# Kernel optimization log

Hardware: AMD Instinct MI355X
Metric: run time of the kernel (lower is better)

Reference implementation:

```python
import jax, jax.numpy as jnp
import numpy as np

NUM_HEADS = 16
HIDDEN = 1024
HEAD = HIDDEN // NUM_HEADS

def setup_inputs() -> dict:
    key = jax.random.key(0)
    k1, k2 = jax.random.split(key)
    embeddings = jax.random.normal(k1, (4, 2048, HIDDEN), dtype=jnp.float32)
    w_qkv = jax.random.normal(k2, (HIDDEN, 3 * HIDDEN), dtype=jnp.float32) * (1.0 / np.sqrt(HIDDEN))
    return {"embeddings": embeddings, "w_qkv": w_qkv}

def reference(embeddings, w_qkv):
    b, s, h = embeddings.shape
    # qkv projection (no bias): [b, s, 3*h]
    result = embeddings @ w_qkv
    # split '(qkv nah hdsz)': qkv outermost, then heads, then head dim
    result = result.reshape(b, s, 3, NUM_HEADS, HEAD)
    q = jnp.transpose(result[:, :, 0], (0, 2, 1, 3))  # [b, nah, s, hd]
    k = jnp.transpose(result[:, :, 1], (0, 2, 1, 3))
    v = jnp.transpose(result[:, :, 2], (0, 2, 1, 3))
    # NOTE: original scales by 1/sqrt(hidden_size), not 1/sqrt(head_size)
    scores = jnp.einsum('bnqd,bnkd->bnqk', q, k) / jnp.sqrt(jnp.float32(h))
    probs = jax.nn.softmax(scores, axis=-1)
    ctx = jnp.einsum('bnqk,bnkd->bnqd', probs, v)  # [b, nah, s, hd]
    out = jnp.transpose(ctx, (0, 2, 1, 3)).reshape(b, s, h)
    return out
```

## Files before the change

### kernel.cpp

```cpp
#include <hip/hip_runtime.h>
#include <hip/hip_bf16.h>


typedef __attribute__((ext_vector_type(8))) __bf16 bf16x8;
typedef __attribute__((ext_vector_type(8))) unsigned short u16x8;
typedef __attribute__((ext_vector_type(4))) unsigned short u16x4;
typedef __attribute__((ext_vector_type(4))) float f32x4;

#define B_  4
#define S_  2048
#define H_  1024
#define NH_ 16
#define HD_ 64
#define N3_ 3072
#define M_  (B_*S_)

static __device__ __forceinline__ unsigned short f2bf(float f) {
  __bf16 h = (__bf16)f;
  return __builtin_bit_cast(unsigned short, h);
}

__global__ __launch_bounds__(256) void cvt_emb_kernel(
    const float* __restrict__ in, unsigned short* __restrict__ out, int n4) {
  int i = blockIdx.x * blockDim.x + threadIdx.x;
  int stride = gridDim.x * blockDim.x;
  const float4* in4 = (const float4*)in;
  for (; i < n4; i += stride) {
    float4 v = in4[i];
    ushort4 o;
    o.x = f2bf(v.x); o.y = f2bf(v.y); o.z = f2bf(v.z); o.w = f2bf(v.w);
    ((ushort4*)out)[i] = o;
  }
}

__global__ __launch_bounds__(256) void cvt_w_kernel(
    const float* __restrict__ in, unsigned short* __restrict__ out) {
  __shared__ __align__(16) unsigned short tile[64 * 64];
  const int t = threadIdx.x;
  const int n0 = blockIdx.x * 64;
  const int k0 = blockIdx.y * 64;
#pragma unroll
  for (int it = 0; it < 4; ++it) {
    int c = it * 256 + t;
    int row = c >> 4;
    int a = c & 15;
    float4 v = *(const float4*)(in + (size_t)(k0 + row) * N3_ + n0 + a * 4);
    u16x4 o;
    o[0] = f2bf(v.x); o[1] = f2bf(v.y); o[2] = f2bf(v.z); o[3] = f2bf(v.w);
    int swz = (((row & 7) ^ ((row >> 3) & 7)) << 4);
    *(u16x4*)((char*)tile + row * 128 + ((a * 8) ^ swz)) = o;
  }
  __syncthreads();
#pragma unroll
  for (int it = 0; it < 2; ++it) {
    int c = it * 256 + t;
    int n = c >> 3;
    int a = c & 7;
    u16x8 o;
#pragma unroll
    for (int j = 0; j < 8; ++j) {
      int k = a * 8 + j;
      int swz = (((k & 7) ^ ((k >> 3) & 7)) << 4);
      o[j] = *(const unsigned short*)((char*)tile + k * 128 + ((2 * n) ^ swz));
    }
    *(u16x8*)(out + (size_t)(n0 + n) * H_ + k0 + a * 8) = o;
  }
}

__global__ __launch_bounds__(256) void qkv_gemm_kernel(
    const unsigned short* __restrict__ A,
    const unsigned short* __restrict__ BT,
    unsigned short* __restrict__ C) {
  __shared__ __align__(16) unsigned short a_lds[128 * 64];
  __shared__ __align__(16) unsigned short b_lds[128 * 64];
  const int t = threadIdx.x;
  const int lane = t & 63;
  const int w = t >> 6;
  const int wm = w >> 1, wn = w & 1;
  const int m0 = blockIdx.y * 128;
  const int n0 = blockIdx.x * 128;
  const int lr = lane & 15;
  const int lh = lane >> 4;

  f32x4 acc[4][4];
  for (int i = 0; i < 4; i++)
    for (int j = 0; j < 4; j++)
      for (int r = 0; r < 4; r++) acc[i][j][r] = 0.f;

  for (int kt = 0; kt < 16; ++kt) {
    __syncthreads();
#pragma unroll
    for (int r = 0; r < 4; ++r) {
      int idx = r * 256 + t;
      int row = idx >> 3, ch = idx & 7;
      int sw = (ch * 16) ^ ((row & 7) << 4);
      u16x8 av = *(const u16x8*)(A + (size_t)(m0 + row) * H_ + kt * 64 + ch * 8);
      *(u16x8*)((char*)a_lds + row * 128 + sw) = av;
      u16x8 bv = *(const u16x8*)(BT + (size_t)(n0 + row) * H_ + kt * 64 + ch * 8);
      *(u16x8*)((char*)b_lds + row * 128 + sw) = bv;
    }
    __syncthreads();
#pragma unroll
    for (int kb = 0; kb < 2; ++kb) {
      bf16x8 af[4], bfr[4];
#pragma unroll
      for (int mi = 0; mi < 4; mi++) {
        int row = wm * 64 + mi * 16 + lr;
        int off = (kb * 64 + lh * 16) ^ ((row & 7) << 4);
        af[mi] = *(const bf16x8*)((char*)a_lds + row * 128 + off);
      }
#pragma unroll
      for (int ni = 0; ni < 4; ni++) {
        int row = wn * 64 + ni * 16 + lr;
        int off = (kb * 64 + lh * 16) ^ ((row & 7) << 4);
        bfr[ni] = *(const bf16x8*)((char*)b_lds + row * 128 + off);
      }
#pragma unroll
      for (int mi = 0; mi < 4; mi++)
#pragma unroll
        for (int ni = 0; ni < 4; ni++)
          acc[mi][ni] = __builtin_amdgcn_mfma_f32_16x16x32_bf16(
              af[mi], bfr[ni], acc[mi][ni], 0, 0, 0);
    }
  }
#pragma unroll
  for (int mi = 0; mi < 4; mi++)
#pragma unroll
    for (int ni = 0; ni < 4; ni++)
#pragma unroll
      for (int rg = 0; rg < 4; rg++) {
        int row = m0 + wm * 64 + mi * 16 + lh * 4 + rg;
        int col = n0 + wn * 64 + ni * 16 + lr;
        C[(size_t)row * N3_ + col] = f2bf(acc[mi][ni][rg]);
      }
}

__global__ __launch_bounds__(256) void vtrans_kernel(
    const unsigned short* __restrict__ qkv, unsigned short* __restrict__ vt) {
  __shared__ __align__(16) unsigned short tile[64 * 64];
  const int t = threadIdx.x;
  const int st = blockIdx.x;
  const int h = blockIdx.y;
  const int b = blockIdx.z;
  const int s0 = st * 64;
#pragma unroll
  for (int it = 0; it < 2; ++it) {
    int c = it * 256 + t;
    int row = c >> 3;
    int a = c & 7;
    u16x8 v = *(const u16x8*)(qkv + (size_t)(b * S_ + s0 + row) * N3_ +
                              2 * H_ + h * HD_ + a * 8);
    int swz = (((row & 7) ^ ((row >> 3) & 7)) << 4);
    *(u16x8*)((char*)tile + row * 128 + ((a * 16) ^ swz)) = v;
  }
  __syncthreads();
#pragma unroll
  for (int it = 0; it < 2; ++it) {
    int c = it * 256 + t;
    int d = c >> 3;
    int a = c & 7;
    u16x8 o;
#pragma unroll
    for (int j = 0; j < 8; ++j) {
      int r = a * 8 + j;
      int swz = (((r & 7) ^ ((r >> 3) & 7)) << 4);
      o[j] = *(const unsigned short*)((char*)tile + r * 128 + ((2 * d) ^ swz));
    }
    *(u16x8*)(vt + ((size_t)((b * NH_ + h) * HD_) + d) * S_ + s0 + a * 8) = o;
  }
}

__global__ __launch_bounds__(256) void attn_kernel(
    const unsigned short* __restrict__ QKV,
    const unsigned short* __restrict__ VT,
    float* __restrict__ out) {
  __shared__ __align__(16) unsigned short k_lds[64 * 64];
  __shared__ __align__(16) unsigned short vt_lds[64 * 64];
  const int t = threadIdx.x;
  const int lane = t & 63;
  const int w = t >> 6;
  const int lr = lane & 15, lh = lane >> 4;
  const int qt = blockIdx.x;
  const int h = blockIdx.y;
  const int b = blockIdx.z;
  const int qbase = qt * 64 + w * 16;
  const float scale = 0.03125f;

  bf16x8 qf[2];
  {
    const unsigned short* qp =
        QKV + (size_t)(b * S_ + qbase + lr) * N3_ + h * HD_ + lh * 8;
    qf[0] = *(const bf16x8*)(qp);
    qf[1] = *(const bf16x8*)(qp + 32);
  }

  f32x4 o[4];
#pragma unroll
  for (int i = 0; i < 4; i++)
#pragma unroll
    for (int r = 0; r < 4; r++) o[i][r] = 0.f;
  float mrun = -1e30f, lsum = 0.f;

  const unsigned short* kbase = QKV + (size_t)(b * S_) * N3_ + H_ + h * HD_;
  const unsigned short* vbase = VT + (size_t)((b * NH_ + h) * HD_) * S_;

  for (int kt = 0; kt < 32; ++kt) {
    __syncthreads();
#pragma unroll
    for (int it = 0; it < 2; ++it) {
      int c = it * 256 + t;
      int row = c >> 3, a = c & 7;
      u16x8 kv = *(const u16x8*)(kbase + (size_t)(kt * 64 + row) * N3_ + a * 8);
      *(u16x8*)((char*)k_lds + row * 128 + ((a * 16) ^ ((row & 7) << 4))) = kv;
      u16x8 vv = *(const u16x8*)(vbase + (size_t)row * S_ + kt * 64 + a * 8);
      int s0a = a * 8, s0b = a * 8 + 4;
      int p_lo = ((s0a >> 5) << 3) | (((s0a >> 2) & 3) << 1) | ((s0a >> 4) & 1);
      int p_hi = ((s0b >> 5) << 3) | (((s0b >> 2) & 3) << 1) | ((s0b >> 4) & 1);
      u16x4 lo = {vv[0], vv[1], vv[2], vv[3]};
      u16x4 hi = {vv[4], vv[5], vv[6], vv[7]};
      int rsw = (row & 7) << 4;
      *(u16x4*)((char*)vt_lds + row * 128 + ((p_lo * 8) ^ rsw)) = lo;
      *(u16x4*)((char*)vt_lds + row * 128 + ((p_hi * 8) ^ rsw)) = hi;
    }
    __syncthreads();

    f32x4 sacc[4];
#pragma unroll
    for (int nt = 0; nt < 4; nt++)
#pragma unroll
      for (int r = 0; r < 4; r++) sacc[nt][r] = 0.f;
#pragma unroll
    for (int nt = 0; nt < 4; ++nt) {
#pragma unroll
      for (int kb = 0; kb < 2; ++kb) {
        int row = nt * 16 + lr;
        bf16x8 kf = *(const bf16x8*)((char*)k_lds + row * 128 +
                                     ((64 * kb + 16 * lh) ^ ((row & 7) << 4)));
        sacc[nt] = __builtin_amdgcn_mfma_f32_16x16x32_bf16(kf, qf[kb], sacc[nt], 0, 0, 0);
      }
    }

    float mx = -1e30f;
#pragma unroll
    for (int nt = 0; nt < 4; nt++)
#pragma unroll
      for (int rg = 0; rg < 4; rg++) mx = fmaxf(mx, sacc[nt][rg]);
    mx *= scale;
    mx = fmaxf(mx, __shfl_xor(mx, 16, 64));
    mx = fmaxf(mx, __shfl_xor(mx, 32, 64));
    float mn = fmaxf(mrun, mx);
    float alpha = __expf(mrun - mn);
    mrun = mn;

    float p[4][4];
    float ps = 0.f;
#pragma unroll
    for (int nt = 0; nt < 4; nt++)
#pragma unroll
      for (int rg = 0; rg < 4; rg++) {
        float e = __expf(sacc[nt][rg] * scale - mn);
        p[nt][rg] = e;
        ps += e;
      }
    ps += __shfl_xor(ps, 16, 64);
    ps += __shfl_xor(ps, 32, 64);
    lsum = lsum * alpha + ps;

    bf16x8 pa[2];
#pragma unroll
    for (int kb = 0; kb < 2; ++kb)
#pragma unroll
      for (int j = 0; j < 8; ++j)
        pa[kb][j] = (__bf16)p[2 * kb + (j >> 2)][j & 3];

    float al[4];
#pragma unroll
    for (int rg = 0; rg < 4; ++rg) al[rg] = __shfl(alpha, lh * 4 + rg, 64);
#pragma unroll
    for (int dt = 0; dt < 4; ++dt)
#pragma unroll
      for (int rg = 0; rg < 4; ++rg) o[dt][rg] *= al[rg];

#pragma unroll
    for (int kb = 0; kb < 2; ++kb) {
#pragma unroll
      for (int dt = 0; dt < 4; ++dt) {
        int row = dt * 16 + lr;
        bf16x8 vb = *(const bf16x8*)((char*)vt_lds + row * 128 +
                                     ((64 * kb + 16 * lh) ^ ((row & 7) << 4)));
        o[dt] = __builtin_amdgcn_mfma_f32_16x16x32_bf16(pa[kb], vb, o[dt], 0, 0, 0);
      }
    }
  }

  float ls[4];
#pragma unroll
  for (int rg = 0; rg < 4; ++rg) ls[rg] = __shfl(lsum, lh * 4 + rg, 64);
#pragma unroll
  for (int dt = 0; dt < 4; ++dt)
#pragma unroll
    for (int rg = 0; rg < 4; ++rg) {
      int qrow = qbase + lh * 4 + rg;
      out[(size_t)(b * S_ + qrow) * H_ + h * HD_ + dt * 16 + lr] =
          o[dt][rg] / ls[rg];
    }
}

extern "C" void kernel_launch(void* const* d_in, const int* in_sizes, int n_in,
                              void* d_out, int out_size, void* d_ws, size_t ws_size,
                              hipStream_t stream) {
  const float* emb = (const float*)d_in[0];
  const float* wqkv = (const float*)d_in[1];
  float* out = (float*)d_out;

  unsigned short* abf = (unsigned short*)d_ws;
  unsigned short* wtb = abf + (size_t)M_ * H_;
  unsigned short* qkv = wtb + (size_t)N3_ * H_;
  unsigned short* vt = abf;

  cvt_emb_kernel<<<dim3(2048), dim3(256), 0, stream>>>(emb, abf, (M_ * H_) / 4);
  cvt_w_kernel<<<dim3(48, 16), dim3(256), 0, stream>>>(wqkv, wtb);
  qkv_gemm_kernel<<<dim3(N3_ / 128, M_ / 128), dim3(256), 0, stream>>>(abf, wtb, qkv);
  vtrans_kernel<<<dim3(32, 16, 4), dim3(256), 0, stream>>>(qkv, vt);
  attn_kernel<<<dim3(32, 16, 4), dim3(256), 0, stream>>>(qkv, vt, out);
}
```

Measured before the change: 293.2 us.

## Overhaul GEMM loads and attention with register prefetch, lazy rescale, exp2 softmax

The GEMM now fills LDS with direct global-to-LDS loads, and Q is pre-scaled by log2(e)/sqrt(hidden) in the GEMM epilogue so attention can use raw v_exp_f32. V is permuted once in the transpose kernel, so the attention loader is a plain copy. Each attention wave now handles 32 query rows, with the next K/V tile prefetched into registers. The running-max rescale is skipped while the max grows by at most 8, and the row sum comes from an MFMA against a ones vector instead of shuffles. These changes target LDS store overhead, global-load latency, and exp/reduction ALU work, at the cost of higher register pressure and bf16 rounding of the pre-scaled Q.

```diff
diff --git a/kernel.cpp b/kernel.cpp
--- a/kernel.cpp
+++ b/kernel.cpp
@@ -18,6 +18,17 @@
 static __device__ __forceinline__ unsigned short f2bf(float f) {
   __bf16 h = (__bf16)f;
   return __builtin_bit_cast(unsigned short, h);
+}
+
+static __device__ __forceinline__ float exp2_fast(float x) {
+  float r; asm("v_exp_f32 %0, %1" : "=v"(r) : "v"(x)); return r;
+}
+
+static __device__ __forceinline__ void gload_lds16(const unsigned short* g,
+                                                   unsigned short* l) {
+  __builtin_amdgcn_global_load_lds(
+      (const __attribute__((address_space(1))) unsigned int*)g,
+      (__attribute__((address_space(3))) unsigned int*)l, 16, 0, 0);
 }
 
 __global__ __launch_bounds__(256) void cvt_emb_kernel(
@@ -67,7 +78,7 @@
   }
 }
 
-__global__ __launch_bounds__(256) void qkv_gemm_kernel(
+__global__ __launch_bounds__(256, 3) void qkv_gemm_kernel(
     const unsigned short* __restrict__ A,
     const unsigned short* __restrict__ BT,
     unsigned short* __restrict__ C) {
@@ -81,23 +92,28 @@
   const int n0 = blockIdx.x * 128;
   const int lr = lane & 15;
   const int lh = lane >> 4;
+  const int sr8 = lane >> 3;
+  const int sch = (lane & 7) ^ sr8;
 
   f32x4 acc[4][4];
+#pragma unroll
   for (int i = 0; i < 4; i++)
+#pragma unroll
     for (int j = 0; j < 4; j++)
+#pragma unroll
       for (int r = 0; r < 4; r++) acc[i][j][r] = 0.f;
+
+  const unsigned short* Abase = A + (size_t)(m0 + w * 32 + sr8) * H_ + sch * 8;
+  const unsigned short* Bbase = BT + (size_t)(n0 + w * 32 + sr8) * H_ + sch * 8;
 
   for (int kt = 0; kt < 16; ++kt) {
     __syncthreads();
 #pragma unroll
-    for (int r = 0; r < 4; ++r) {
-      int idx = r * 256 + t;
-      int row = idx >> 3, ch = idx & 7;
-      int sw = (ch * 16) ^ ((row & 7) << 4);
-      u16x8 av = *(const u16x8*)(A + (size_t)(m0 + row) * H_ + kt * 64 + ch * 8);
-      *(u16x8*)((char*)a_lds + row * 128 + sw) = av;
-      u16x8 bv = *(const u16x8*)(BT + (size_t)(n0 + row) * H_ + kt * 64 + ch * 8);
-      *(u16x8*)((char*)b_lds + row * 128 + sw) = bv;
+    for (int i = 0; i < 4; ++i) {
+      gload_lds16(Abase + (size_t)(i * 8) * H_ + kt * 64,
+                  &a_lds[(w * 32 + i * 8) * 64]);
+      gload_lds16(Bbase + (size_t)(i * 8) * H_ + kt * 64,
+                  &b_lds[(w * 32 + i * 8) * 64]);
     }
     __syncthreads();
 #pragma unroll
@@ -123,6 +139,7 @@
               af[mi], bfr[ni], acc[mi][ni], 0, 0, 0);
     }
   }
+  const float mult = (n0 < H_) ? 0.045084220027780106f : 1.0f;
 #pragma unroll
   for (int mi = 0; mi < 4; mi++)
 #pragma unroll
@@ -131,7 +148,7 @@
       for (int rg = 0; rg < 4; rg++) {
         int row = m0 + wm * 64 + mi * 16 + lh * 4 + rg;
         int col = n0 + wn * 64 + ni * 16 + lr;
-        C[(size_t)row * N3_ + col] = f2bf(acc[mi][ni][rg]);
+        C[(size_t)row * N3_ + col] = f2bf(acc[mi][ni][rg] * mult);
       }
 }
 
@@ -166,11 +183,19 @@
       int swz = (((r & 7) ^ ((r >> 3) & 7)) << 4);
       o[j] = *(const unsigned short*)((char*)tile + r * 128 + ((2 * d) ^ swz));
     }
-    *(u16x8*)(vt + ((size_t)((b * NH_ + h) * HD_) + d) * S_ + s0 + a * 8) = o;
-  }
-}
-
-__global__ __launch_bounds__(256) void attn_kernel(
+    int s0a = a * 8, s0b = a * 8 + 4;
+    int p_lo = ((s0a >> 5) << 3) | (((s0a >> 2) & 3) << 1) | ((s0a >> 4) & 1);
+    int p_hi = ((s0b >> 5) << 3) | (((s0b >> 2) & 3) << 1) | ((s0b >> 4) & 1);
+    unsigned short* dst =
+        vt + ((size_t)((b * NH_ + h) * HD_) + d) * S_ + s0;
+    u16x4 lo = {o[0], o[1], o[2], o[3]};
+    u16x4 hi = {o[4], o[5], o[6], o[7]};
+    *(u16x4*)(dst + p_lo * 4) = lo;
+    *(u16x4*)(dst + p_hi * 4) = hi;
+  }
+}
+
+__global__ __launch_bounds__(256, 3) void attn_kernel(
     const unsigned short* __restrict__ QKV,
     const unsigned short* __restrict__ VT,
     float* __restrict__ out) {
@@ -180,55 +205,72 @@
   const int lane = t & 63;
   const int w = t >> 6;
   const int lr = lane & 15, lh = lane >> 4;
-  const int qt = blockIdx.x;
   const int h = blockIdx.y;
   const int b = blockIdx.z;
-  const int qbase = qt * 64 + w * 16;
-  const float scale = 0.03125f;
-
-  bf16x8 qf[2];
-  {
+  const int qw = blockIdx.x * 128 + w * 32;
+
+  bf16x8 qf[2][2];
+#pragma unroll
+  for (int qi = 0; qi < 2; ++qi) {
     const unsigned short* qp =
-        QKV + (size_t)(b * S_ + qbase + lr) * N3_ + h * HD_ + lh * 8;
-    qf[0] = *(const bf16x8*)(qp);
-    qf[1] = *(const bf16x8*)(qp + 32);
-  }
-
-  f32x4 o[4];
-#pragma unroll
-  for (int i = 0; i < 4; i++)
-#pragma unroll
-    for (int r = 0; r < 4; r++) o[i][r] = 0.f;
-  float mrun = -1e30f, lsum = 0.f;
-
+        QKV + (size_t)(b * S_ + qw + qi * 16 + lr) * N3_ + h * HD_ + lh * 8;
+    qf[qi][0] = *(const bf16x8*)qp;
+    qf[qi][1] = *(const bf16x8*)(qp + 32);
+  }
+
+  bf16x8 ones;
+#pragma unroll
+  for (int j = 0; j < 8; ++j) ones[j] = (lr == 0) ? (__bf16)1.0f : (__bf16)0.0f;
+
+  f32x4 o[2][4], o5[2];
+#pragma unroll
+  for (int qi = 0; qi < 2; ++qi) {
+#pragma unroll
+    for (int i = 0; i < 4; i++)
+#pragma unroll
+      for (int r = 0; r < 4; r++) o[qi][i][r] = 0.f;
+#pragma unroll
+    for (int r = 0; r < 4; r++) o5[qi][r] = 0.f;
+  }
+  float mrun[2] = {-3e38f, -3e38f};
+
+  const int row0 = t >> 3, a0 = t & 7;
+  const int row1 = (256 + t) >> 3, a1 = t & 7;
+  const int dst0 = row0 * 128 + ((a0 * 16) ^ ((row0 & 7) << 4));
+  const int dst1 = row1 * 128 + ((a1 * 16) ^ ((row1 & 7) << 4));
   const unsigned short* kbase = QKV + (size_t)(b * S_) * N3_ + H_ + h * HD_;
   const unsigned short* vbase = VT + (size_t)((b * NH_ + h) * HD_) * S_;
 
+  u16x8 gk0 = *(const u16x8*)(kbase + (size_t)row0 * N3_ + a0 * 8);
+  u16x8 gk1 = *(const u16x8*)(kbase + (size_t)row1 * N3_ + a1 * 8);
+  u16x8 gv0 = *(const u16x8*)(vbase + (size_t)row0 * S_ + a0 * 8);
+  u16x8 gv1 = *(const u16x8*)(vbase + (size_t)row1 * S_ + a1 * 8);
+
   for (int kt = 0; kt < 32; ++kt) {
     __syncthreads();
-#pragma unroll
-    for (int it = 0; it < 2; ++it) {
-      int c = it * 256 + t;
-      int row = c >> 3, a = c & 7;
-      u16x8 kv = *(const u16x8*)(kbase + (size_t)(kt * 64 + row) * N3_ + a * 8);
-      *(u16x8*)((char*)k_lds + row * 128 + ((a * 16) ^ ((row & 7) << 4))) = kv;
-      u16x8 vv = *(const u16x8*)(vbase + (size_t)row * S_ + kt * 64 + a * 8);
-      int s0a = a * 8, s0b = a * 8 + 4;
-      int p_lo = ((s0a >> 5) << 3) | (((s0a >> 2) & 3) << 1) | ((s0a >> 4) & 1);
-      int p_hi = ((s0b >> 5) << 3) | (((s0b >> 2) & 3) << 1) | ((s0b >> 4) & 1);
-      u16x4 lo = {vv[0], vv[1], vv[2], vv[3]};
-      u16x4 hi = {vv[4], vv[5], vv[6], vv[7]};
-      int rsw = (row & 7) << 4;
-      *(u16x4*)((char*)vt_lds + row * 128 + ((p_lo * 8) ^ rsw)) = lo;
-      *(u16x4*)((char*)vt_lds + row * 128 + ((p_hi * 8) ^ rsw)) = hi;
-    }
+    *(u16x8*)((char*)k_lds + dst0) = gk0;
+    *(u16x8*)((char*)k_lds + dst1) = gk1;
+    *(u16x8*)((char*)vt_lds + dst0) = gv0;
+    *(u16x8*)((char*)vt_lds + dst1) = gv1;
     __syncthreads();
 
-    f32x4 sacc[4];
-#pragma unroll
-    for (int nt = 0; nt < 4; nt++)
-#pragma unroll
-      for (int r = 0; r < 4; r++) sacc[nt][r] = 0.f;
+    {
+      int ktn = (kt + 1) & 31;
+      const unsigned short* kp = kbase + (size_t)(ktn * 64) * N3_;
+      const unsigned short* vp = vbase + ktn * 64;
+      gk0 = *(const u16x8*)(kp + (size_t)row0 * N3_ + a0 * 8);
+      gk1 = *(const u16x8*)(kp + (size_t)row1 * N3_ + a1 * 8);
+      gv0 = *(const u16x8*)(vp + (size_t)row0 * S_ + a0 * 8);
+      gv1 = *(const u16x8*)(vp + (size_t)row1 * S_ + a1 * 8);
+    }
+
+    f32x4 sacc[2][4];
+#pragma unroll
+    for (int qi = 0; qi < 2; ++qi)
+#pragma unroll
+      for (int nt = 0; nt < 4; nt++)
+#pragma unroll
+        for (int r = 0; r < 4; r++) sacc[qi][nt][r] = 0.f;
 #pragma unroll
     for (int nt = 0; nt < 4; ++nt) {
 #pragma unroll
@@ -236,50 +278,56 @@
         int row = nt * 16 + lr;
         bf16x8 kf = *(const bf16x8*)((char*)k_lds + row * 128 +
                                      ((64 * kb + 16 * lh) ^ ((row & 7) << 4)));
-        sacc[nt] = __builtin_amdgcn_mfma_f32_16x16x32_bf16(kf, qf[kb], sacc[nt], 0, 0, 0);
-      }
-    }
-
-    float mx = -1e30f;
-#pragma unroll
-    for (int nt = 0; nt < 4; nt++)
-#pragma unroll
-      for (int rg = 0; rg < 4; rg++) mx = fmaxf(mx, sacc[nt][rg]);
-    mx *= scale;
-    mx = fmaxf(mx, __shfl_xor(mx, 16, 64));
-    mx = fmaxf(mx, __shfl_xor(mx, 32, 64));
-    float mn = fmaxf(mrun, mx);
-    float alpha = __expf(mrun - mn);
-    mrun = mn;
-
-    float p[4][4];
-    float ps = 0.f;
-#pragma unroll
-    for (int nt = 0; nt < 4; nt++)
-#pragma unroll
-      for (int rg = 0; rg < 4; rg++) {
-        float e = __expf(sacc[nt][rg] * scale - mn);
-        p[nt][rg] = e;
-        ps += e;
-      }
-    ps += __shfl_xor(ps, 16, 64);
-    ps += __shfl_xor(ps, 32, 64);
-    lsum = lsum * alpha + ps;
-
-    bf16x8 pa[2];
-#pragma unroll
-    for (int kb = 0; kb < 2; ++kb)
-#pragma unroll
-      for (int j = 0; j < 8; ++j)
-        pa[kb][j] = (__bf16)p[2 * kb + (j >> 2)][j & 3];
-
-    float al[4];
-#pragma unroll
-    for (int rg = 0; rg < 4; ++rg) al[rg] = __shfl(alpha, lh * 4 + rg, 64);
-#pragma unroll
-    for (int dt = 0; dt < 4; ++dt)
-#pragma unroll
-      for (int rg = 0; rg < 4; ++rg) o[dt][rg] *= al[rg];
+        sacc[0][nt] = __builtin_amdgcn_mfma_f32_16x16x32_bf16(kf, qf[0][kb], sacc[0][nt], 0, 0, 0);
+        sacc[1][nt] = __builtin_amdgcn_mfma_f32_16x16x32_bf16(kf, qf[1][kb], sacc[1][nt], 0, 0, 0);
+      }
+    }
+
+    float mx[2];
+#pragma unroll
+    for (int qi = 0; qi < 2; ++qi) {
+      float m = fmaxf(fmaxf(fmaxf(sacc[qi][0][0], sacc[qi][0][1]),
+                            fmaxf(sacc[qi][0][2], sacc[qi][0][3])),
+                      fmaxf(fmaxf(sacc[qi][1][0], sacc[qi][1][1]),
+                            fmaxf(sacc[qi][1][2], sacc[qi][1][3])));
+      float m2 = fmaxf(fmaxf(fmaxf(sacc[qi][2][0], sacc[qi][2][1]),
+                             fmaxf(sacc[qi][2][2], sacc[qi][2][3])),
+                       fmaxf(fmaxf(sacc[qi][3][0], sacc[qi][3][1]),
+                             fmaxf(sacc[qi][3][2], sacc[qi][3][3])));
+      m = fmaxf(m, m2);
+      m = fmaxf(m, __shfl_xor(m, 16, 64));
+      m = fmaxf(m, __shfl_xor(m, 32, 64));
+      mx[qi] = m;
+    }
+
+    bool ok = (mx[0] <= mrun[0] + 8.0f) && (mx[1] <= mrun[1] + 8.0f);
+    if (!__all(ok)) {
+#pragma unroll
+      for (int qi = 0; qi < 2; ++qi) {
+        float mn = fmaxf(mrun[qi], mx[qi]);
+        float alpha = exp2_fast(mrun[qi] - mn);
+        mrun[qi] = mn;
+        float al[4];
+#pragma unroll
+        for (int rg = 0; rg < 4; ++rg) al[rg] = __shfl(alpha, lh * 4 + rg, 64);
+#pragma unroll
+        for (int dt = 0; dt < 4; ++dt)
+#pragma unroll
+          for (int rg = 0; rg < 4; ++rg) o[qi][dt][rg] *= al[rg];
+#pragma unroll
+        for (int rg = 0; rg < 4; ++rg) o5[qi][rg] *= al[rg];
+      }
+    }
+
+    bf16x8 pa[2][2];
+#pragma unroll
+    for (int qi = 0; qi < 2; ++qi)
+#pragma unroll
+      for (int kb = 0; kb < 2; ++kb)
+#pragma unroll
+        for (int j = 0; j < 8; ++j)
+          pa[qi][kb][j] =
+              (__bf16)exp2_fast(sacc[qi][2 * kb + (j >> 2)][j & 3] - mrun[qi]);
 
 #pragma unroll
     for (int kb = 0; kb < 2; ++kb) {
@@ -288,22 +336,31 @@
         int row = dt * 16 + lr;
         bf16x8 vb = *(const bf16x8*)((char*)vt_lds + row * 128 +
                                      ((64 * kb + 16 * lh) ^ ((row & 7) << 4)));
-        o[dt] = __builtin_amdgcn_mfma_f32_16x16x32_bf16(pa[kb], vb, o[dt], 0, 0, 0);
-      }
-    }
-  }
-
-  float ls[4];
-#pragma unroll
-  for (int rg = 0; rg < 4; ++rg) ls[rg] = __shfl(lsum, lh * 4 + rg, 64);
-#pragma unroll
-  for (int dt = 0; dt < 4; ++dt)
+        o[0][dt] = __builtin_amdgcn_mfma_f32_16x16x32_bf16(pa[0][kb], vb, o[0][dt], 0, 0, 0);
+        o[1][dt] = __builtin_amdgcn_mfma_f32_16x16x32_bf16(pa[1][kb], vb, o[1][dt], 0, 0, 0);
+      }
+      o5[0] = __builtin_amdgcn_mfma_f32_16x16x32_bf16(pa[0][kb], ones, o5[0], 0, 0, 0);
+      o5[1] = __builtin_amdgcn_mfma_f32_16x16x32_bf16(pa[1][kb], ones, o5[1], 0, 0, 0);
+    }
+  }
+
+#pragma unroll
+  for (int qi = 0; qi < 2; ++qi) {
+    float inv[4];
 #pragma unroll
     for (int rg = 0; rg < 4; ++rg) {
-      int qrow = qbase + lh * 4 + rg;
-      out[(size_t)(b * S_ + qrow) * H_ + h * HD_ + dt * 16 + lr] =
-          o[dt][rg] / ls[rg];
-    }
+      float ls = __shfl(o5[qi][rg], lh * 16, 64);
+      inv[rg] = 1.0f / ls;
+    }
+#pragma unroll
+    for (int dt = 0; dt < 4; ++dt)
+#pragma unroll
+      for (int rg = 0; rg < 4; ++rg) {
+        int qrow = qw + qi * 16 + lh * 4 + rg;
+        out[(size_t)(b * S_ + qrow) * H_ + h * HD_ + dt * 16 + lr] =
+            o[qi][dt][rg] * inv[rg];
+      }
+  }
 }
 
 extern "C" void kernel_launch(void* const* d_in, const int* in_sizes, int n_in,
@@ -322,5 +379,5 @@
   cvt_w_kernel<<<dim3(48, 16), dim3(256), 0, stream>>>(wqkv, wtb);
   qkv_gemm_kernel<<<dim3(N3_ / 128, M_ / 128), dim3(256), 0, stream>>>(abf, wtb, qkv);
   vtrans_kernel<<<dim3(32, 16, 4), dim3(256), 0, stream>>>(qkv, vt);
-  attn_kernel<<<dim3(32, 16, 4), dim3(256), 0, stream>>>(qkv, vt, out);
-}
+  attn_kernel<<<dim3(16, 16, 4), dim3(256), 0, stream>>>(qkv, vt, out);
+}
```

Measured after the change: 248.4 us. 1.18x faster.
